# Kernel tuning notes

Hardware: AMD Instinct MI355X
Metric: run time of the kernel (lower is better)

## Reference

```python
import jax, jax.numpy as jnp
import numpy as np

DIM = 512
HEADS = 8
DIM_HEAD = 64
INNER = HEADS * DIM_HEAD  # 512
B, N = 32, 512
LN_EPS = 1e-5


def setup_inputs() -> dict:
    key = jax.random.key(0)
    ks = jax.random.split(key, 8)
    inp = {
        "q": jax.random.normal(ks[0], (B, N, DIM), jnp.float32),
        "k": jax.random.normal(ks[1], (B, N, DIM), jnp.float32),
        "v": jax.random.normal(ks[2], (B, N, DIM), jnp.float32),
        "ln_w": jnp.ones((DIM,), jnp.float32),
        "ln_b": jnp.zeros((DIM,), jnp.float32),
        "W_in": jax.random.normal(ks[3], (DIM, INNER), jnp.float32) / np.sqrt(DIM),
        "W_out": jax.random.normal(ks[4], (INNER, DIM), jnp.float32) / np.sqrt(INNER),
        "b_out": jnp.zeros((DIM,), jnp.float32),
        "cov_w_raw": jnp.float32(0.6),
        "var_w_raw": jnp.float32(0.2),
    }
    return inp


def _project(x, ln_w, ln_b, W_in):
    # LayerNorm(dim) -> Linear(dim, inner, bias=False) -> 'b n (h d) -> h b n d'
    mu = jnp.mean(x, axis=-1, keepdims=True)
    var = jnp.var(x, axis=-1, keepdims=True)  # biased, as in nn.LayerNorm
    xn = (x - mu) / jnp.sqrt(var + LN_EPS) * ln_w + ln_b
    f = xn @ W_in  # [B, N, inner]
    Bq, Nq, _ = f.shape
    f = f.reshape(Bq, Nq, HEADS, DIM_HEAD)
    return jnp.transpose(f, (2, 0, 1, 3))  # [h, B, N, d]


def reference(q, k, v, ln_w, ln_b, W_in, W_out, b_out, cov_w_raw, var_w_raw):
    f_q = _project(q, ln_w, ln_b, W_in)  # [h, B, N, d]
    f_k = _project(k, ln_w, ln_b, W_in)
    f_v = _project(v, ln_w, ln_b, W_in)

    d = f_q.shape[-1]

    # cosine similarity: (q . k) / (||q|| ||k||)
    dots = jnp.einsum('hbnd,hbmd->hbnm', f_q, f_k)
    qn = jnp.linalg.norm(f_q, axis=-1)  # [h, B, N]
    kn = jnp.linalg.norm(f_k, axis=-1)  # [h, B, M]
    cosine_sim = dots / (qn[..., :, None] * kn[..., None, :])

    # basic covariance component: centered dot / d
    qc = f_q - jnp.mean(f_q, axis=-1, keepdims=True)
    kc = f_k - jnp.mean(f_k, axis=-1, keepdims=True)
    cov_component = jnp.einsum('hbnd,hbmd->hbnm', qc, kc) / d

    # variance component: outer product of per-token variances (unbiased) / d
    q_var = jnp.var(f_q, axis=-1, ddof=1)  # [h, B, N]
    k_var = jnp.var(f_k, axis=-1, ddof=1)  # [h, B, M]
    var_component = (q_var[..., :, None] * k_var[..., None, :]) / d

    cov_w = jax.nn.sigmoid(cov_w_raw)
    var_w = jax.nn.sigmoid(var_w_raw)
    cos_w = 1.0 - cov_w - var_w

    scores = cos_w * cosine_sim + cov_w * cov_component + var_w * var_component
    out = jnp.einsum('hbnm,hbmd->hbnd', scores, f_v)  # no softmax in cosine variant

    # 'h b n d -> b n (h d)'
    out = jnp.transpose(out, (1, 2, 0, 3)).reshape(out.shape[1], out.shape[2], INNER)
    return out @ W_out + b_out
```

## Files before the change

kernel.cpp:

```cpp
#include <hip/hip_runtime.h>
#include <stdint.h>

using u16 = unsigned short;
using u32 = unsigned int;
using bf16x8 = __bf16 __attribute__((ext_vector_type(8)));
using f32x4  = float __attribute__((ext_vector_type(4)));

__device__ __forceinline__ float bflo(u32 u){ return __uint_as_float(u << 16); }
__device__ __forceinline__ float bfhi(u32 u){ return __uint_as_float(u & 0xffff0000u); }
__device__ __forceinline__ u16 f2bf(float f){
  u32 u = __float_as_uint(f);
  u += 0x7fffu + ((u >> 16) & 1u);
  return (u16)(u >> 16);
}
__device__ __forceinline__ u32 pk2(float a, float b){
  u32 r;
  asm("v_cvt_pk_bf16_f32 %0, %1, %2" : "=v"(r) : "v"(a), "v"(b));
  return r;
}
__device__ __forceinline__ void gload16(const void* g, void* l){
  __builtin_amdgcn_global_load_lds(
      (const __attribute__((address_space(1))) void*)(uintptr_t)(g),
      (__attribute__((address_space(3))) void*)(uintptr_t)(l), 16, 0, 0);
}

__global__ __launch_bounds__(256) void prep_k(const float* __restrict__ Win,
                                              const float* __restrict__ Wout,
                                              const float* __restrict__ lnw,
                                              const float* __restrict__ lnb,
                                              u16* __restrict__ WpT,
                                              u16* __restrict__ WoutT,
                                              float* __restrict__ g1,
                                              float* __restrict__ g2){
  __shared__ float tile[32][33];
  __shared__ float red[2][8][32];
  int bid = blockIdx.x;
  if (bid < 512){
    int bz = bid >> 8, bi = bid & 255;
    int bx = bi & 15, by = bi >> 4;
    const float* src = bz ? Wout : Win;
    u16* dst = bz ? WoutT : WpT;
    int tx = threadIdx.x & 31, ty = threadIdx.x >> 5;
    int c0 = bx * 32, r0 = by * 32;
#pragma unroll
    for (int i = 0; i < 4; ++i)
      tile[ty + i*8][tx] = src[(size_t)(r0 + ty + i*8)*512 + c0 + tx];
    __syncthreads();
    float sc = bz ? 1.f : lnw[r0 + tx];
#pragma unroll
    for (int i = 0; i < 4; ++i)
      dst[(size_t)(c0 + ty + i*8)*512 + r0 + tx] = f2bf(tile[tx][ty + i*8] * sc);
  } else {
    int bi = bid - 512;
    int col = bi*32 + (threadIdx.x & 31);
    int s = threadIdx.x >> 5;
    float p1 = 0.f, p2 = 0.f;
    for (int kk = 0; kk < 64; ++kk){
      int k = s*64 + kk;
      float wv = Win[(size_t)k*512 + col];
      p1 += lnw[k]*wv; p2 += lnb[k]*wv;
    }
    red[0][s][threadIdx.x & 31] = p1;
    red[1][s][threadIdx.x & 31] = p2;
    __syncthreads();
    if (threadIdx.x < 32){
      float a1 = 0.f, a2 = 0.f;
#pragma unroll
      for (int s2 = 0; s2 < 8; ++s2){ a1 += red[0][s2][threadIdx.x]; a2 += red[1][s2][threadIdx.x]; }
      g1[bi*32 + threadIdx.x] = a1;
      g2[bi*32 + threadIdx.x] = a2;
    }
  }
}

template<int ORIENT, int FSTAT>
__device__ __forceinline__ void proj_body(
    const float* __restrict__ X, const u16* __restrict__ Wp,
    const float* __restrict__ g1, const float* __restrict__ g2,
    u16* __restrict__ C, float* __restrict__ fstat, int ldC, int bid,
    char* sW, char* sX, float* sF){
  float* sMu = sF;        float* sRs = sF + 128;
  float* sG1 = sF + 256;  float* sG2 = sF + 384;
  const int t = threadIdx.x, w = t >> 6, l = t & 63;
  const int wr = w >> 1, wc = w & 1;
  const int lr = l & 15, lg = l >> 4;
  int bx, by;
  if (ORIENT == 0){ bx = bid & 127; by = bid >> 7; }
  else { int j = bid >> 3; bx = j & 3; by = (bid & 7) + 8*(j >> 2); }
  const int row0 = bx * 128, col0 = by * 128;
  const int xbase = (ORIENT == 0) ? row0 : col0;
  const int wbase = (ORIENT == 0) ? col0 : row0;

  const int sc = t >> 3, k8 = t & 7;
  const int sso = (k8*16) ^ ((sc & 7) << 4);
  const char* Wpp = (const char*)Wp + ((size_t)(wbase + sc) << 10) + sso;
  const float* Xp = X + ((size_t)(xbase + sc) << 9) + k8*8;

  if (t < 128){ sG1[t] = g1[wbase + t]; sG2[t] = g2[wbase + t]; }

  float xr[4][8];
  float psum[4] = {}, pss[4] = {};
  f32x4 acc[4][4] = {};

  auto XLOAD = [&](int kt){
#pragma unroll
    for (int ii = 0; ii < 4; ++ii){
      const float* p = Xp + ii*(32*512) + kt*64;
      float4 a = *(const float4*)p, c4 = *(const float4*)(p + 4);
      xr[ii][0]=a.x;  xr[ii][1]=a.y;  xr[ii][2]=a.z;  xr[ii][3]=a.w;
      xr[ii][4]=c4.x; xr[ii][5]=c4.y; xr[ii][6]=c4.z; xr[ii][7]=c4.w;
    }
  };
  auto XWRITE = [&](){
#pragma unroll
    for (int ii = 0; ii < 4; ++ii){
#pragma unroll
      for (int e = 0; e < 8; ++e){ psum[ii] += xr[ii][e]; pss[ii] += xr[ii][e]*xr[ii][e]; }
      uint4 pk;
      pk.x = pk2(xr[ii][0], xr[ii][1]); pk.y = pk2(xr[ii][2], xr[ii][3]);
      pk.z = pk2(xr[ii][4], xr[ii][5]); pk.w = pk2(xr[ii][6], xr[ii][7]);
      *(uint4*)(sX + (sc + ii*32)*128 + sso) = pk;
    }
  };
  auto WSTAGE = [&](int kt){
#pragma unroll
    for (int ii = 0; ii < 4; ++ii)
      gload16(Wpp + (size_t)ii*32768 + kt*128, sW + ii*4096 + w*1024);
  };

  XLOAD(0);
  for (int kt = 0; kt < 8; ++kt){
    WSTAGE(kt);
    XWRITE();
    asm volatile("s_waitcnt vmcnt(0) lgkmcnt(0)" ::: "memory");
    __builtin_amdgcn_s_barrier();
    __builtin_amdgcn_sched_barrier(0);
    if (kt < 7) XLOAD(kt + 1);
    __builtin_amdgcn_sched_barrier(0);
    const char* aB = (ORIENT == 0) ? sX : sW;
    const char* bB = (ORIENT == 0) ? sW : sX;
#pragma unroll
    for (int kk = 0; kk < 2; ++kk){
      bf16x8 af[4], bfg[4];
#pragma unroll
      for (int m = 0; m < 4; ++m){
        int r = wr*64 + m*16 + lr;
        af[m] = *(const bf16x8*)(aB + r*128 + ((kk*64 + lg*16) ^ ((r & 7) << 4)));
      }
#pragma unroll
      for (int n = 0; n < 4; ++n){
        int r = wc*64 + n*16 + lr;
        bfg[n] = *(const bf16x8*)(bB + r*128 + ((kk*64 + lg*16) ^ ((r & 7) << 4)));
      }
#pragma unroll
      for (int m = 0; m < 4; ++m)
#pragma unroll
        for (int n = 0; n < 4; ++n)
          acc[m][n] = __builtin_amdgcn_mfma_f32_16x16x32_bf16(af[m], bfg[n], acc[m][n], 0, 0, 0);
    }
    asm volatile("s_waitcnt lgkmcnt(0)" ::: "memory");
    __builtin_amdgcn_s_barrier();
    __builtin_amdgcn_sched_barrier(0);
  }

#pragma unroll
  for (int ii = 0; ii < 4; ++ii){
    float s = psum[ii], s2 = pss[ii];
#pragma unroll
    for (int off = 1; off < 8; off <<= 1){ s += __shfl_xor(s, off); s2 += __shfl_xor(s2, off); }
    if (k8 == 0){
      float mu = s * (1.f/512.f);
      sMu[sc + ii*32] = mu;
      sRs[sc + ii*32] = rsqrtf(s2 * (1.f/512.f) - mu*mu + 1e-5f);
    }
  }
  __syncthreads();

  float cs[4] = {}, cs2[4] = {};
#pragma unroll
  for (int m = 0; m < 4; ++m){
#pragma unroll
    for (int q = 0; q < 4; ++q){
      int ri = wr*64 + m*16 + lg*4 + q;
      float rsv = 0.f, muv = 0.f, g1r = 0.f, g2r = 0.f;
      if (ORIENT == 0){ rsv = sRs[ri]; muv = sMu[ri]; }
      else { g1r = sG1[ri]; g2r = sG2[ri]; }
      float fv[4];
#pragma unroll
      for (int n = 0; n < 4; ++n){
        int ci = wc*64 + n*16 + lr;
        float a = acc[m][n][q];
        if (ORIENT == 0) fv[n] = rsv*(a - muv*sG1[ci]) + sG2[ci];
        else             fv[n] = sRs[ci]*(a - sMu[ci]*g1r) + g2r;
        C[(size_t)(row0 + ri)*ldC + (col0 + ci)] = f2bf(fv[n]);
        if (FSTAT == 2){ cs[n] += fv[n]; cs2[n] += fv[n]*fv[n]; }
      }
      if (FSTAT == 1){
        float s  = (fv[0]+fv[1]) + (fv[2]+fv[3]);
        float s2 = (fv[0]*fv[0]+fv[1]*fv[1]) + (fv[2]*fv[2]+fv[3]*fv[3]);
#pragma unroll
        for (int off = 1; off < 16; off <<= 1){ s += __shfl_xor(s, off); s2 += __shfl_xor(s2, off); }
        if (lr == 0){
          int head = (col0 >> 6) + wc;
          *(float2*)(fstat + ((size_t)(row0 + ri)*8 + head)*2) = make_float2(s, s2);
        }
      }
    }
  }
  if (FSTAT == 2){
    int head = (row0 >> 6) + wr;
#pragma unroll
    for (int n = 0; n < 4; ++n){
      float s = cs[n], s2 = cs2[n];
      s += __shfl_xor(s, 16); s2 += __shfl_xor(s2, 16);
      s += __shfl_xor(s, 32); s2 += __shfl_xor(s2, 32);
      if (lg == 0){
        int tok = col0 + wc*64 + n*16 + lr;
        *(float2*)(fstat + ((size_t)tok*8 + head)*2) = make_float2(s, s2);
      }
    }
  }
}

__global__ __launch_bounds__(256, 3) void proj_k(
    const float* __restrict__ q, const float* __restrict__ k, const float* __restrict__ v,
    const u16* __restrict__ Wp, const float* __restrict__ g1, const float* __restrict__ g2,
    u16* __restrict__ fq, u16* __restrict__ kT, u16* __restrict__ vT,
    float* __restrict__ qstat, float* __restrict__ kstat){
  __shared__ __align__(16) char sW[16384];
  __shared__ __align__(16) char sX[16384];
  __shared__ float sF[512];
  int bid = blockIdx.x;
  if (bid < 512)
    proj_body<0,1>(q, Wp, g1, g2, fq, qstat, 512, bid, sW, sX, sF);
  else if (bid < 1024)
    proj_body<1,2>(k, Wp, g1, g2, kT, kstat, 16384, bid - 512, sW, sX, sF);
  else
    proj_body<1,0>(v, Wp, g1, g2, vT, nullptr, 16384, bid - 1024, sW, sX, sF);
}

__global__ __launch_bounds__(256) void outgemm_k(
    const u16* __restrict__ A, const u16* __restrict__ B,
    float* __restrict__ Cf, const float* __restrict__ bias){
  __shared__ __align__(16) char sM[65536];
  const int t = threadIdx.x, w = t >> 6, l = t & 63;
  const int wr = w >> 1, wc = w & 1;
  const int lr = l & 15, lg = l >> 4;
  const int bx = blockIdx.x & 127, by = blockIdx.x >> 7;
  const int row0 = bx*128, col0 = by*128;

  const int spr = t >> 3, se = (t & 7) ^ (spr & 7);
  const int srow = spr*2 + (se >> 2), sk16 = se & 3;
  const char* Ap0 = (const char*)A + ((size_t)(row0 + srow) << 10) + sk16*16;
  const char* Bp0 = (const char*)B + ((size_t)(col0 + srow) << 10) + sk16*16;
  const int ldst = w*1024 + l*16;

  const int qf = ((((lr & 1) << 2) | lg) ^ ((lr >> 1) & 7)) * 16;
  const int afb = wr*4096 + (lr >> 1)*128 + qf;
  const int bfb = wc*4096 + (lr >> 1)*128 + qf;

  f32x4 acc[4][4] = {};

  auto STAGE = [&](int kt, int buf){
    char* d = sM + buf*16384;
    gload16(Ap0 + kt*64,         d + ldst);
    gload16(Ap0 + 65536 + kt*64, d + 4096 + ldst);
    gload16(Bp0 + kt*64,         d + 8192 + ldst);
    gload16(Bp0 + 65536 + kt*64, d + 12288 + ldst);
  };

  STAGE(0, 0); STAGE(1, 1); STAGE(2, 2);
#pragma unroll
  for (int kt = 0; kt < 16; ++kt){
    if (kt < 14)       asm volatile("s_waitcnt vmcnt(8)" ::: "memory");
    else if (kt == 14) asm volatile("s_waitcnt vmcnt(4)" ::: "memory");
    else               asm volatile("s_waitcnt vmcnt(0)" ::: "memory");
    __builtin_amdgcn_s_barrier();
    __builtin_amdgcn_sched_barrier(0);
    if (kt < 13) STAGE(kt + 3, (kt + 3) & 3);
    const char* aR = sM + (kt & 3)*16384;
    const char* bR = aR + 8192;
    bf16x8 af[4], bfg[4];
#pragma unroll
    for (int m = 0; m < 4; ++m) af[m]  = *(const bf16x8*)(aR + afb + m*1024);
#pragma unroll
    for (int n = 0; n < 4; ++n) bfg[n] = *(const bf16x8*)(bR + bfb + n*1024);
#pragma unroll
    for (int m = 0; m < 4; ++m)
#pragma unroll
      for (int n = 0; n < 4; ++n)
        acc[m][n] = __builtin_amdgcn_mfma_f32_16x16x32_bf16(af[m], bfg[n], acc[m][n], 0, 0, 0);
  }

#pragma unroll
  for (int m = 0; m < 4; ++m){
#pragma unroll
    for (int qq = 0; qq < 4; ++qq){
      int r = row0 + wr*64 + m*16 + lg*4 + qq;
#pragma unroll
      for (int n = 0; n < 4; ++n){
        int cc = col0 + wc*64 + n*16 + lr;
        Cf[(size_t)r*512 + cc] = acc[m][n][qq] + bias[cc];
      }
    }
  }
}

__global__ __launch_bounds__(512) void attn_k(
    const u16* __restrict__ fq, const u16* __restrict__ kT, const u16* __restrict__ vT,
    const float* __restrict__ qstat, const float* __restrict__ kstat,
    u16* __restrict__ ao,
    const float* __restrict__ cwr, const float* __restrict__ vwr){
  __shared__ __align__(16) char smem[131072 + 1664*4];
  float* sStat = (float*)(smem + 131072);
  float* sS1 = sStat + 1536;
  float* sS2 = sStat + 1600;

  const int t = threadIdx.x, w = t >> 6, l = t & 63;
  const int lr = l & 15, lg = l >> 4;
  const int h = blockIdx.x & 7, b = blockIdx.x >> 3;

  float cwv = 1.f/(1.f + __expf(-*cwr));
  float vwv = 1.f/(1.f + __expf(-*vwr));
  float cosw = 1.f - cwv - vwv;

  const char* kTb = (const char*)kT + (size_t)h*64*32768 + (size_t)b*1024;
  const char* vTb = (const char*)vT + (size_t)h*64*32768 + (size_t)b*1024;
#pragma unroll
  for (int ii = 0; ii < 8; ++ii){
    int c = ii*512 + t, d = c >> 6, u = c & 63;
    int so = d*32768 + ((u ^ (d & 7)) << 4);
    gload16(kTb + so, smem + ii*8192 + w*1024);
    gload16(vTb + so, smem + 65536 + ii*8192 + w*1024);
  }
  {
    float2 ksr = *(const float2*)(kstat + ((size_t)(b*512 + t)*8 + h)*2);
    float mk = ksr.x * (1.f/64.f);
    sStat[t]        = rsqrtf(ksr.y);
    sStat[512 + t]  = mk;
    sStat[1024 + t] = (ksr.y - 64.f*mk*mk) * (1.f/63.f);
  }
  __syncthreads();

  const int jt = (w >> 1), itp = (w & 1);
  f32x4 m2acc[2] = {}, m1acc[2] = {};
  {
    const int j = jt*16 + lr;
#pragma unroll
    for (int ks = 0; ks < 16; ++ks){
      int u = ks*4 + lg;
      bf16x8 af = *(const bf16x8*)(smem + 65536 + j*1024 + ((u ^ (j & 7)) << 4));
#pragma unroll
      for (int tt = 0; tt < 2; ++tt){
        int i = (itp*2 + tt)*16 + lr;
        bf16x8 bf = *(const bf16x8*)(smem + i*1024 + ((u ^ (i & 7)) << 4));
        m2acc[tt] = __builtin_amdgcn_mfma_f32_16x16x32_bf16(af, bf, m2acc[tt], 0, 0, 0);
      }
    }
  }
  {
    int j = t >> 3, g = t & 7;
    float p1 = 0.f, p2 = 0.f;
#pragma unroll
    for (int uu = 0; uu < 8; ++uu){
      int ut = g*8 + uu;
      uint4 uv = *(const uint4*)(smem + 65536 + j*1024 + ((ut ^ (j & 7)) << 4));
      int m0 = ut*8;
      float4 mk0 = *(const float4*)(sStat + 512 + m0);
      float4 mk1 = *(const float4*)(sStat + 512 + m0 + 4);
      float4 kv0 = *(const float4*)(sStat + 1024 + m0);
      float4 kv1 = *(const float4*)(sStat + 1024 + m0 + 4);
      float v0=bflo(uv.x),v1=bfhi(uv.x),v2=bflo(uv.y),v3=bfhi(uv.y);
      float v4=bflo(uv.z),v5=bfhi(uv.z),v6=bflo(uv.w),v7=bfhi(uv.w);
      p1 += v0*mk0.x + v1*mk0.y + v2*mk0.z + v3*mk0.w
          + v4*mk1.x + v5*mk1.y + v6*mk1.z + v7*mk1.w;
      p2 += v0*kv0.x + v1*kv0.y + v2*kv0.z + v3*kv0.w
          + v4*kv1.x + v5*kv1.y + v6*kv1.z + v7*kv1.w;
    }
#pragma unroll
    for (int off = 1; off < 8; off <<= 1){ p1 += __shfl_xor(p1, off); p2 += __shfl_xor(p2, off); }
    if (g == 0){ sS1[j] = p1; sS2[j] = p2; }
  }
  __syncthreads();

#pragma unroll
  for (int ii = 0; ii < 32; ++ii){
    int wd = ii*512 + t;
    int d = wd >> 8, o = wd & 255, ud = o >> 2, p = o & 3;
    int m0 = ((ud ^ (d & 7)) << 3) + p*2;
    u32 uv = *(u32*)(smem + wd*4);
    *(u32*)(smem + wd*4) = pk2(bflo(uv)*sStat[m0], bfhi(uv)*sStat[m0+1]);
  }
  __syncthreads();

  {
    const int j = jt*16 + lr;
#pragma unroll
    for (int ks = 0; ks < 16; ++ks){
      int u = ks*4 + lg;
      bf16x8 af = *(const bf16x8*)(smem + 65536 + j*1024 + ((u ^ (j & 7)) << 4));
#pragma unroll
      for (int tt = 0; tt < 2; ++tt){
        int i = (itp*2 + tt)*16 + lr;
        bf16x8 bf = *(const bf16x8*)(smem + i*1024 + ((u ^ (i & 7)) << 4));
        m1acc[tt] = __builtin_amdgcn_mfma_f32_16x16x32_bf16(af, bf, m1acc[tt], 0, 0, 0);
      }
    }
  }
  __syncthreads();

#pragma unroll
  for (int tt = 0; tt < 2; ++tt){
#pragma unroll
    for (int q = 0; q < 4; ++q){
      int j = jt*16 + lg*4 + q;
      int i = (itp*2 + tt)*16 + lr;
      int bo = j*128 + (((i >> 3) ^ (j & 7)) << 4) + (i & 7)*2;
      *(u16*)(smem + bo)        = f2bf(m1acc[tt][q]);
      *(u16*)(smem + 8192 + bo) = f2bf(m2acc[tt][q]);
    }
  }
  const char* fqb = (const char*)fq + (size_t)b*524288 + h*128;
#pragma unroll
  for (int ii = 0; ii < 8; ++ii){
    int c = ii*512 + t, n = c >> 3, u = c & 7;
    gload16(fqb + n*1024 + ((u ^ (n & 7)) << 4), smem + 65536 + ii*8192 + w*1024);
  }
  __syncthreads();

  float s1v[4], s2v[4];
#pragma unroll
  for (int nt = 0; nt < 4; ++nt){ s1v[nt] = sS1[nt*16 + lr]; s2v[nt] = sS2[nt*16 + lr]; }
  const float Bc = cwv * (1.f/64.f);

#pragma unroll
  for (int mt = 0; mt < 4; ++mt){
    f32x4 a1[4] = {}, a2[4] = {};
    const int n = w*64 + mt*16 + lr;
#pragma unroll
    for (int kk = 0; kk < 2; ++kk){
      int u = kk*4 + lg;
      bf16x8 af = *(const bf16x8*)(smem + 65536 + n*128 + ((u ^ (n & 7)) << 4));
#pragma unroll
      for (int nt = 0; nt < 4; ++nt){
        int j = nt*16 + lr;
        bf16x8 b1 = *(const bf16x8*)(smem + j*128 + ((u ^ (j & 7)) << 4));
        bf16x8 b2 = *(const bf16x8*)(smem + 8192 + j*128 + ((u ^ (j & 7)) << 4));
        a1[nt] = __builtin_amdgcn_mfma_f32_16x16x32_bf16(af, b1, a1[nt], 0, 0, 0);
        a2[nt] = __builtin_amdgcn_mfma_f32_16x16x32_bf16(af, b2, a2[nt], 0, 0, 0);
      }
    }
#pragma unroll
    for (int q = 0; q < 4; ++q){
      int nr = w*64 + mt*16 + lg*4 + q;
      float2 qs = *(const float2*)(qstat + ((size_t)(b*512 + nr)*8 + h)*2);
      float mq = qs.x * (1.f/64.f);
      float An = cosw * rsqrtf(qs.y);
      float Cn = -cwv * mq;
      float En = vwv * (1.f/64.f) * ((qs.y - 64.f*mq*mq) * (1.f/63.f));
      char* op = (char*)ao + ((size_t)(b*512 + nr)*512 + h*64)*2;
#pragma unroll
      for (int nt = 0; nt < 4; ++nt){
        float ov = An*a1[nt][q] + Bc*a2[nt][q] + Cn*s1v[nt] + En*s2v[nt];
        *(u16*)(op + (nt*16 + lr)*2) = f2bf(ov);
      }
    }
  }
}

extern "C" void kernel_launch(void* const* d_in, const int* in_sizes, int n_in,
                              void* d_out, int out_size, void* d_ws, size_t ws_size,
                              hipStream_t stream){
  const float* q    = (const float*)d_in[0];
  const float* k    = (const float*)d_in[1];
  const float* v    = (const float*)d_in[2];
  const float* lnw  = (const float*)d_in[3];
  const float* lnb  = (const float*)d_in[4];
  const float* Win  = (const float*)d_in[5];
  const float* Wout = (const float*)d_in[6];
  const float* bout = (const float*)d_in[7];
  const float* cwr  = (const float*)d_in[8];
  const float* vwr  = (const float*)d_in[9];

  char* ws = (char*)d_ws;
  const size_t FB = (size_t)16384 * 512 * 2;
  u16* fq  = (u16*)(ws);
  u16* kT  = (u16*)(ws + FB);
  u16* vT  = (u16*)(ws + 2*FB);
  u16* ao  = (u16*)(ws + 3*FB);
  u16* WpT   = (u16*)(ws + 4*FB);
  u16* WoutT = (u16*)(ws + 4*FB + 524288);
  float* g1  = (float*)(ws + 4*FB + 1048576);
  float* g2  = (float*)(ws + 4*FB + 1048576 + 2048);
  float* qstat = (float*)d_out;
  float* kstat = qstat + 262144;

  prep_k<<<528, 256, 0, stream>>>(Win, Wout, lnw, lnb, WpT, WoutT, g1, g2);

  proj_k<<<1536, 256, 0, stream>>>(q, k, v, WpT, g1, g2, fq, kT, vT, qstat, kstat);

  attn_k<<<256, 512, 0, stream>>>(fq, kT, vT, qstat, kstat, ao, cwr, vwr);

  outgemm_k<<<512, 256, 0, stream>>>(ao, WoutT, (float*)d_out, bout);
}
```

Measured before the change: 95.57 us.

## Double-buffer weight tiles in LDS and prefetch activations two stages ahead

The projection GEMM loop now keeps two shared-memory buffers for the weight tiles. The next tile is staged asynchronously while the MFMAs consume the current one, and activation rows are prefetched into two register slots two k-steps ahead. A partial vmcnt wait replaces the full drain, and the k-loop is fully unrolled. The bf16 pack helper also switches from the hardware packed-convert instruction to software round-to-nearest-even. This costs more VALU work, a larger LDS footprint (48KB for sW plus sX) and extra registers under a 3-blocks-per-CU bound.

Result: slower. 325.3 us (median of 2 runs) (+240.4%).

```diff
diff --git a/kernel.cpp b/kernel.cpp
--- a/kernel.cpp
+++ b/kernel.cpp
@@ -14,9 +14,7 @@
   return (u16)(u >> 16);
 }
 __device__ __forceinline__ u32 pk2(float a, float b){
-  u32 r;
-  asm("v_cvt_pk_bf16_f32 %0, %1, %2" : "=v"(r) : "v"(a), "v"(b));
-  return r;
+  return (u32)f2bf(a) | ((u32)f2bf(b) << 16);
 }
 __device__ __forceinline__ void gload16(const void* g, void* l){
   __builtin_amdgcn_global_load_lds(
@@ -98,47 +96,52 @@
 
   if (t < 128){ sG1[t] = g1[wbase + t]; sG2[t] = g2[wbase + t]; }
 
-  float xr[4][8];
+  float xr[2][4][8];
   float psum[4] = {}, pss[4] = {};
   f32x4 acc[4][4] = {};
 
-  auto XLOAD = [&](int kt){
+  auto XLOAD = [&](int kt, int slot){
 #pragma unroll
     for (int ii = 0; ii < 4; ++ii){
       const float* p = Xp + ii*(32*512) + kt*64;
       float4 a = *(const float4*)p, c4 = *(const float4*)(p + 4);
-      xr[ii][0]=a.x;  xr[ii][1]=a.y;  xr[ii][2]=a.z;  xr[ii][3]=a.w;
-      xr[ii][4]=c4.x; xr[ii][5]=c4.y; xr[ii][6]=c4.z; xr[ii][7]=c4.w;
+      xr[slot][ii][0]=a.x;  xr[slot][ii][1]=a.y;  xr[slot][ii][2]=a.z;  xr[slot][ii][3]=a.w;
+      xr[slot][ii][4]=c4.x; xr[slot][ii][5]=c4.y; xr[slot][ii][6]=c4.z; xr[slot][ii][7]=c4.w;
     }
   };
-  auto XWRITE = [&](){
+  auto XWRITE = [&](int slot){
 #pragma unroll
     for (int ii = 0; ii < 4; ++ii){
 #pragma unroll
-      for (int e = 0; e < 8; ++e){ psum[ii] += xr[ii][e]; pss[ii] += xr[ii][e]*xr[ii][e]; }
+      for (int e = 0; e < 8; ++e){ psum[ii] += xr[slot][ii][e]; pss[ii] += xr[slot][ii][e]*xr[slot][ii][e]; }
       uint4 pk;
-      pk.x = pk2(xr[ii][0], xr[ii][1]); pk.y = pk2(xr[ii][2], xr[ii][3]);
-      pk.z = pk2(xr[ii][4], xr[ii][5]); pk.w = pk2(xr[ii][6], xr[ii][7]);
+      pk.x = pk2(xr[slot][ii][0], xr[slot][ii][1]); pk.y = pk2(xr[slot][ii][2], xr[slot][ii][3]);
+      pk.z = pk2(xr[slot][ii][4], xr[slot][ii][5]); pk.w = pk2(xr[slot][ii][6], xr[slot][ii][7]);
       *(uint4*)(sX + (sc + ii*32)*128 + sso) = pk;
     }
   };
-  auto WSTAGE = [&](int kt){
+  auto WSTAGE = [&](int kt, int buf){
 #pragma unroll
     for (int ii = 0; ii < 4; ++ii)
-      gload16(Wpp + (size_t)ii*32768 + kt*128, sW + ii*4096 + w*1024);
+      gload16(Wpp + (size_t)ii*32768 + kt*128, sW + buf*16384 + ii*4096 + w*1024);
   };
 
-  XLOAD(0);
+  XLOAD(0, 0);
+  WSTAGE(0, 0);
+  XLOAD(1, 1);
+#pragma unroll
   for (int kt = 0; kt < 8; ++kt){
-    WSTAGE(kt);
-    XWRITE();
-    asm volatile("s_waitcnt vmcnt(0) lgkmcnt(0)" ::: "memory");
+    XWRITE(kt & 1);
+    if (kt < 7) asm volatile("s_waitcnt vmcnt(8) lgkmcnt(0)" ::: "memory");
+    else        asm volatile("s_waitcnt vmcnt(0) lgkmcnt(0)" ::: "memory");
     __builtin_amdgcn_s_barrier();
     __builtin_amdgcn_sched_barrier(0);
-    if (kt < 7) XLOAD(kt + 1);
+    if (kt < 7) WSTAGE(kt + 1, (kt + 1) & 1);
+    if (kt < 6) XLOAD(kt + 2, kt & 1);
     __builtin_amdgcn_sched_barrier(0);
-    const char* aB = (ORIENT == 0) ? sX : sW;
-    const char* bB = (ORIENT == 0) ? sW : sX;
+    const char* wB = sW + (kt & 1)*16384;
+    const char* aB = (ORIENT == 0) ? sX : wB;
+    const char* bB = (ORIENT == 0) ? wB : sX;
 #pragma unroll
     for (int kk = 0; kk < 2; ++kk){
       bf16x8 af[4], bfg[4];
@@ -227,7 +230,7 @@
     const u16* __restrict__ Wp, const float* __restrict__ g1, const float* __restrict__ g2,
     u16* __restrict__ fq, u16* __restrict__ kT, u16* __restrict__ vT,
     float* __restrict__ qstat, float* __restrict__ kstat){
-  __shared__ __align__(16) char sW[16384];
+  __shared__ __align__(16) char sW[32768];
   __shared__ __align__(16) char sX[16384];
   __shared__ float sF[512];
   int bid = blockIdx.x;
```

## Halve projection K-tile to 32, shrink LDS, raise occupancy to 5 blocks

Applied to the files above, without the earlier changes.

Cuts the projection GEMM's K-tile from 64 to 32, so the loop runs 16 iterations and each block stages half as much W and X in LDS. Thread-to-row mapping, swizzle and per-row LayerNorm stat reduction are reworked to match, and launch bounds go from 3 to 5 blocks per CU. The aim is higher occupancy and better latency hiding, at the cost of twice as many barriers per tile. The bf16 pack also moves from the hardware cvt_pk instruction to a software round-to-nearest-even routine, which costs extra ALU work.

Result: slower. 293.1 us (+206.7%).

```diff
diff --git a/kernel.cpp b/kernel.cpp
--- a/kernel.cpp
+++ b/kernel.cpp
@@ -14,9 +14,7 @@
   return (u16)(u >> 16);
 }
 __device__ __forceinline__ u32 pk2(float a, float b){
-  u32 r;
-  asm("v_cvt_pk_bf16_f32 %0, %1, %2" : "=v"(r) : "v"(a), "v"(b));
-  return r;
+  return (u32)f2bf(a) | ((u32)f2bf(b) << 16);
 }
 __device__ __forceinline__ void gload16(const void* g, void* l){
   __builtin_amdgcn_global_load_lds(
@@ -91,87 +89,83 @@
   const int xbase = (ORIENT == 0) ? row0 : col0;
   const int wbase = (ORIENT == 0) ? col0 : row0;
 
-  const int sc = t >> 3, k8 = t & 7;
-  const int sso = (k8*16) ^ ((sc & 7) << 4);
-  const char* Wpp = (const char*)Wp + ((size_t)(wbase + sc) << 10) + sso;
-  const float* Xp = X + ((size_t)(xbase + sc) << 9) + k8*8;
+  const int sc = t >> 1, hk = t & 1;
+  const float* Xp = X + ((size_t)(xbase + sc) << 9) + hk*16;
+  const int wrow = t >> 2, k16 = t & 3;
+  const char* Wpp = (const char*)Wp + ((size_t)(wbase + wrow) << 10)
+                    + ((k16 ^ ((wrow >> 1) & 3)) << 4);
 
   if (t < 128){ sG1[t] = g1[wbase + t]; sG2[t] = g2[wbase + t]; }
 
-  float xr[4][8];
-  float psum[4] = {}, pss[4] = {};
+  float xr[16];
+  float psum = 0.f, pss = 0.f;
   f32x4 acc[4][4] = {};
 
   auto XLOAD = [&](int kt){
-#pragma unroll
-    for (int ii = 0; ii < 4; ++ii){
-      const float* p = Xp + ii*(32*512) + kt*64;
-      float4 a = *(const float4*)p, c4 = *(const float4*)(p + 4);
-      xr[ii][0]=a.x;  xr[ii][1]=a.y;  xr[ii][2]=a.z;  xr[ii][3]=a.w;
-      xr[ii][4]=c4.x; xr[ii][5]=c4.y; xr[ii][6]=c4.z; xr[ii][7]=c4.w;
-    }
+    const float* p = Xp + kt*32;
+    float4 a = *(const float4*)p,       b4 = *(const float4*)(p + 4);
+    float4 c4 = *(const float4*)(p + 8), d4 = *(const float4*)(p + 12);
+    xr[0]=a.x;  xr[1]=a.y;  xr[2]=a.z;  xr[3]=a.w;
+    xr[4]=b4.x; xr[5]=b4.y; xr[6]=b4.z; xr[7]=b4.w;
+    xr[8]=c4.x; xr[9]=c4.y; xr[10]=c4.z; xr[11]=c4.w;
+    xr[12]=d4.x; xr[13]=d4.y; xr[14]=d4.z; xr[15]=d4.w;
   };
   auto XWRITE = [&](){
 #pragma unroll
-    for (int ii = 0; ii < 4; ++ii){
-#pragma unroll
-      for (int e = 0; e < 8; ++e){ psum[ii] += xr[ii][e]; pss[ii] += xr[ii][e]*xr[ii][e]; }
-      uint4 pk;
-      pk.x = pk2(xr[ii][0], xr[ii][1]); pk.y = pk2(xr[ii][2], xr[ii][3]);
-      pk.z = pk2(xr[ii][4], xr[ii][5]); pk.w = pk2(xr[ii][6], xr[ii][7]);
-      *(uint4*)(sX + (sc + ii*32)*128 + sso) = pk;
-    }
+    for (int e = 0; e < 16; ++e){ psum += xr[e]; pss += xr[e]*xr[e]; }
+    uint4 pa, pb;
+    pa.x = pk2(xr[0], xr[1]);  pa.y = pk2(xr[2], xr[3]);
+    pa.z = pk2(xr[4], xr[5]);  pa.w = pk2(xr[6], xr[7]);
+    pb.x = pk2(xr[8], xr[9]);  pb.y = pk2(xr[10], xr[11]);
+    pb.z = pk2(xr[12], xr[13]); pb.w = pk2(xr[14], xr[15]);
+    int swz = (sc >> 1) & 3;
+    *(uint4*)(sX + sc*64 + (((hk*2)     ^ swz) << 4)) = pa;
+    *(uint4*)(sX + sc*64 + (((hk*2 + 1) ^ swz) << 4)) = pb;
   };
   auto WSTAGE = [&](int kt){
-#pragma unroll
-    for (int ii = 0; ii < 4; ++ii)
-      gload16(Wpp + (size_t)ii*32768 + kt*128, sW + ii*4096 + w*1024);
+    gload16(Wpp + kt*64,         sW + t*16);
+    gload16(Wpp + 65536 + kt*64, sW + 4096 + t*16);
   };
 
   XLOAD(0);
-  for (int kt = 0; kt < 8; ++kt){
+  for (int kt = 0; kt < 16; ++kt){
     WSTAGE(kt);
     XWRITE();
     asm volatile("s_waitcnt vmcnt(0) lgkmcnt(0)" ::: "memory");
     __builtin_amdgcn_s_barrier();
     __builtin_amdgcn_sched_barrier(0);
-    if (kt < 7) XLOAD(kt + 1);
+    if (kt < 15) XLOAD(kt + 1);
     __builtin_amdgcn_sched_barrier(0);
     const char* aB = (ORIENT == 0) ? sX : sW;
     const char* bB = (ORIENT == 0) ? sW : sX;
-#pragma unroll
-    for (int kk = 0; kk < 2; ++kk){
-      bf16x8 af[4], bfg[4];
-#pragma unroll
-      for (int m = 0; m < 4; ++m){
-        int r = wr*64 + m*16 + lr;
-        af[m] = *(const bf16x8*)(aB + r*128 + ((kk*64 + lg*16) ^ ((r & 7) << 4)));
-      }
-#pragma unroll
-      for (int n = 0; n < 4; ++n){
-        int r = wc*64 + n*16 + lr;
-        bfg[n] = *(const bf16x8*)(bB + r*128 + ((kk*64 + lg*16) ^ ((r & 7) << 4)));
-      }
-#pragma unroll
-      for (int m = 0; m < 4; ++m)
-#pragma unroll
-        for (int n = 0; n < 4; ++n)
-          acc[m][n] = __builtin_amdgcn_mfma_f32_16x16x32_bf16(af[m], bfg[n], acc[m][n], 0, 0, 0);
-    }
+    bf16x8 af[4], bfg[4];
+#pragma unroll
+    for (int m = 0; m < 4; ++m){
+      int r = wr*64 + m*16 + lr;
+      af[m] = *(const bf16x8*)(aB + r*64 + ((lg ^ ((r >> 1) & 3)) << 4));
+    }
+#pragma unroll
+    for (int n = 0; n < 4; ++n){
+      int r = wc*64 + n*16 + lr;
+      bfg[n] = *(const bf16x8*)(bB + r*64 + ((lg ^ ((r >> 1) & 3)) << 4));
+    }
+#pragma unroll
+    for (int m = 0; m < 4; ++m)
+#pragma unroll
+      for (int n = 0; n < 4; ++n)
+        acc[m][n] = __builtin_amdgcn_mfma_f32_16x16x32_bf16(af[m], bfg[n], acc[m][n], 0, 0, 0);
     asm volatile("s_waitcnt lgkmcnt(0)" ::: "memory");
     __builtin_amdgcn_s_barrier();
     __builtin_amdgcn_sched_barrier(0);
   }
 
-#pragma unroll
-  for (int ii = 0; ii < 4; ++ii){
-    float s = psum[ii], s2 = pss[ii];
-#pragma unroll
-    for (int off = 1; off < 8; off <<= 1){ s += __shfl_xor(s, off); s2 += __shfl_xor(s2, off); }
-    if (k8 == 0){
+  {
+    float s  = psum + __shfl_xor(psum, 1);
+    float s2 = pss  + __shfl_xor(pss, 1);
+    if (hk == 0){
       float mu = s * (1.f/512.f);
-      sMu[sc + ii*32] = mu;
-      sRs[sc + ii*32] = rsqrtf(s2 * (1.f/512.f) - mu*mu + 1e-5f);
+      sMu[sc] = mu;
+      sRs[sc] = rsqrtf(s2 * (1.f/512.f) - mu*mu + 1e-5f);
     }
   }
   __syncthreads();
@@ -222,13 +216,13 @@
   }
 }
 
-__global__ __launch_bounds__(256, 3) void proj_k(
+__global__ __launch_bounds__(256, 5) void proj_k(
     const float* __restrict__ q, const float* __restrict__ k, const float* __restrict__ v,
     const u16* __restrict__ Wp, const float* __restrict__ g1, const float* __restrict__ g2,
     u16* __restrict__ fq, u16* __restrict__ kT, u16* __restrict__ vT,
     float* __restrict__ qstat, float* __restrict__ kstat){
-  __shared__ __align__(16) char sW[16384];
-  __shared__ __align__(16) char sX[16384];
+  __shared__ __align__(16) char sW[8192];
+  __shared__ __align__(16) char sX[8192];
   __shared__ float sF[512];
   int bid = blockIdx.x;
   if (bid < 512)
```
